# Kernel optimization log

Hardware: AMD Instinct MI355X
Metric: run time of the kernel (lower is better)

## Reference

```python
import jax, jax.numpy as jnp
import numpy as np

D = 4; R = 12; C = 32
P = 2 * R + 1            # 25 fine patch
N = P * P                # 625
MEM_R = 12; MEM_P = 2 * MEM_R + 1
K = 20; DIL_INT = 16


def local_correlation(ft, fr, rad, dil):
    """Zero-padded local correlation (SpatialCorrelationSampler, kernel=1).
    ft, fr: (b,c,h,w) -> (b,Pp,Pp,h,w) with Pp=2*rad+1, patch dilation dil."""
    b, c, h, w = ft.shape
    Pp = 2 * rad + 1
    pad = rad * dil
    frp = jnp.pad(fr, ((0, 0), (0, 0), (pad, pad), (pad, pad)))
    rows = (jnp.arange(Pp)[:, None] * dil + jnp.arange(h)[None, :]).reshape(-1)
    cols = (jnp.arange(Pp)[:, None] * dil + jnp.arange(w)[None, :]).reshape(-1)
    g = frp[:, :, rows, :][:, :, :, cols].reshape(b, c, Pp, h, Pp, w)
    return jnp.einsum('bchw,bcyhxw->byxhw', ft, g)


def bilinear_sample(img, py, px):
    """Bilinear sample img (b,c,H,W) at float coords py/px (broadcastable shape S);
    zero outside the image. Returns (b,c,*S)."""
    b, c, H, W = img.shape
    y0f = jnp.floor(py); x0f = jnp.floor(px)
    wy = py - y0f; wx = px - x0f
    y0 = y0f.astype(jnp.int32); x0 = x0f.astype(jnp.int32)

    def tap(yi, xi, wgt):
        valid = (yi >= 0) & (yi < H) & (xi >= 0) & (xi < W)
        v = img[:, :, jnp.clip(yi, 0, H - 1), jnp.clip(xi, 0, W - 1)]
        return v * (wgt * valid)[None, None]

    return (tap(y0, x0, (1 - wy) * (1 - wx)) + tap(y0, x0 + 1, (1 - wy) * wx)
            + tap(y0 + 1, x0, wy * (1 - wx)) + tap(y0 + 1, x0 + 1, wy * wx))


def _topk_dim1(corr, k):
    # corr: (b,N,hw); torch.topk(dim=1, sorted=True) equivalent
    vals, idx = jax.lax.top_k(corr.transpose(0, 2, 1), k)   # (b,hw,k)
    return vals.transpose(0, 2, 1), idx                      # (b,k,hw), (b,hw,k)


def _long_ref(ft, fr, q, dirate):
    b, c, h, w = ft.shape
    # coarse dilated correlation -> softmax -> soft-argmax expected offset
    corr_c = local_correlation(ft, fr, MEM_R, dirate).reshape(b, MEM_P * MEM_P, h * w)
    attn = jax.nn.softmax(corr_c, axis=1).reshape(b, MEM_P, MEM_P, h, w)
    d = jnp.arange(-MEM_R, MEM_R + 1, dtype=ft.dtype)
    off_y = jnp.einsum('byxhw,y->bhw', attn, d) * dirate
    off_x = jnp.einsum('byxhw,x->bhw', attn, d) * dirate
    # deform_im2col with PxP kernel: sample fr at (r+dy+off_y, c+dx+off_x)
    dtap = jnp.arange(-R, R + 1, dtype=ft.dtype)
    py = dtap[:, None, None, None] + (jnp.arange(h, dtype=ft.dtype)[:, None] + off_y[0])[None, None]
    px = dtap[None, :, None, None] + (jnp.arange(w, dtype=ft.dtype)[None, :] + off_x[0])[None, None]
    col = bilinear_sample(fr, py, px)                        # (b,c,P,P,h,w)
    corr = jnp.einsum('bchw,bcyxhw->byxhw', ft, col).reshape(b, N, h * w)
    vals, idx = _topk_dim1(corr, K)
    # process_long_image_uf_topk: shift offsets by decoded top-k displacement, 1-tap bilinear
    dr = (idx[0] // 25 - 12).reshape(h, w, K).transpose(2, 0, 1).astype(ft.dtype)  # (K,h,w)
    dc = (idx[0] % 25 - 12).reshape(h, w, K).transpose(2, 0, 1).astype(ft.dtype)
    py2 = jnp.arange(h, dtype=ft.dtype)[None, :, None] + off_y[0][None] + dr
    px2 = jnp.arange(w, dtype=ft.dtype)[None, None, :] + off_x[0][None] + dc
    imgs = bilinear_sample(q, py2, px2)                      # (b,C,K,h,w)
    return vals, imgs.reshape(b, q.shape[1], K, h * w)


def _short_ref(ft, fr, q):
    b, c, h, w = ft.shape
    corr = local_correlation(ft, fr, R, 1).reshape(b, N, h * w)
    vals, idx = _topk_dim1(corr, K)
    # process_short_image_uf_topk: integer gather q[:, :, r+dr, c+dc] (zero-padded)
    dr = (idx[0] // 25 - 12).reshape(h, w, K).transpose(2, 0, 1)   # (K,h,w) int
    dc = (idx[0] % 25 - 12).reshape(h, w, K).transpose(2, 0, 1)
    qp = jnp.pad(q, ((0, 0), (0, 0), (R, R), (R, R)))
    yi = jnp.arange(h)[None, :, None] + dr + R
    xi = jnp.arange(w)[None, None, :] + dc + R
    imgs = qp[:, :, yi, xi]                                  # (b,C,K,h,w)
    return vals, imgs.reshape(b, q.shape[1], K, h * w)


def _forward(feats_r, feats_t, quantized_r, ref_index, current_ind):
    ref_index = np.asarray(ref_index)
    current_ind = int(current_ind)
    gaps = current_ind - ref_index
    nsearch = int(np.sum(gaps > DIL_INT))
    dirates = [int(min(4, g // DIL_INT + 1)) for g in gaps if g > DIL_INT]
    nref = feats_r.shape[0]
    b, c, h, w = feats_t.shape
    # prep(): subsample labels by D (C=32 channels, one_hot skipped)
    qr = [quantized_r[i][:, :, ::D, ::D].astype(feats_t.dtype) for i in range(nref)]
    vals_all, imgs_all = [], []
    for i in range(nsearch):
        v, im = _long_ref(feats_t, feats_r[i], qr[i], dirates[i])
        vals_all.append(v); imgs_all.append(im)
    for i in range(nsearch, nref):
        v, im = _short_ref(feats_t, feats_r[i], qr[i])
        vals_all.append(v); imgs_all.append(im)
    attn = jax.nn.softmax(jnp.concatenate(vals_all, axis=1), axis=1)  # (b, nref*K, hw)
    imgs = jnp.concatenate(imgs_all, axis=2)                          # (b, C, nref*K, hw)
    return jnp.einsum('bkp,bckp->bcp', attn, imgs).reshape(b, qr[0].shape[1], h, w)


def setup_inputs():
    key = jax.random.key(0)
    k1, k2, k3 = jax.random.split(key, 3)
    feats_r = jax.random.normal(k1, (3, 1, 64, 48, 48), dtype=jnp.float32)
    feats_t = jax.random.normal(k2, (1, 64, 48, 48), dtype=jnp.float32)
    quantized_r = jax.random.uniform(k3, (3, 1, 32, 192, 192), dtype=jnp.float32)
    # gaps vs current_ind=60: 20 (>16 -> long ref, dirate=2), 10, 5 (short refs)
    ref_index = np.array([40, 50, 55], dtype=np.int64)
    current_ind = 60
    return {"feats_r": feats_r, "feats_t": feats_t, "quantized_r": quantized_r,
            "ref_index": ref_index, "current_ind": current_ind}


def reference(feats_r, feats_t, quantized_r, ref_index, current_ind):
    return _forward(feats_r, feats_t, quantized_r, ref_index, current_ind)
```

## Files before the change

### kernel.cpp

```cpp
#include <hip/hip_runtime.h>
#include <math.h>

#define HW 48
#define NPIX 2304
#define CF 64
#define CQ 32
#define RAD 12
#define PP 25
#define NTAP 625
#define KTOP 20
#define DILINT 16
#define QW 192
#define CSTRIDE 640
#define NPB 6
#define NC 30
#define LROW 68
#define DGS 28


__device__ inline int read_ref_index(const void* rip, int r) {
    const long long* p64 = (const long long*)rip;
    long long v0 = p64[0];
    if (v0 >= 0 && v0 < 1000000) return (int)p64[r];
    return ((const int*)rip)[r];
}

__device__ inline int get_dil(const void* refIdx, const void* curInd, int r,
                              bool* isLong) {
    int cur = ((const int*)curInd)[0];
    int gap = cur - read_ref_index(refIdx, r);
    *isLong = gap > DILINT;
    return *isLong ? min(4, gap / DILINT + 1) : 1;
}

__device__ inline float gather_color(const float* __restrict__ qb, int c,
                                     int y, int x, int id, bool isLong,
                                     float oy, float ox) {
    int dr = id / PP - RAD, dc = id % PP - RAD;
    float img = 0.f;
    if (isLong) {
        float py = (float)y + oy + (float)dr;
        float px = (float)x + ox + (float)dc;
        float fy0 = floorf(py), fx0 = floorf(px);
        int y0 = (int)fy0, x0 = (int)fx0;
        float wy = py - fy0, wx = px - fx0;
        float w00 = (1.f - wy) * (1.f - wx), w01 = (1.f - wy) * wx;
        float w10 = wy * (1.f - wx), w11 = wy * wx;
        if (y0 >= 0 && y0 < HW && x0 >= 0 && x0 < HW)
            img += w00 * qb[(y0 * HW + x0) * CQ + c];
        if (y0 >= 0 && y0 < HW && x0 + 1 >= 0 && x0 + 1 < HW)
            img += w01 * qb[(y0 * HW + x0 + 1) * CQ + c];
        if (y0 + 1 >= 0 && y0 + 1 < HW && x0 >= 0 && x0 < HW)
            img += w10 * qb[((y0 + 1) * HW + x0) * CQ + c];
        if (y0 + 1 >= 0 && y0 + 1 < HW && x0 + 1 >= 0 && x0 + 1 < HW)
            img += w11 * qb[((y0 + 1) * HW + x0 + 1) * CQ + c];
    } else {
        int yy = y + dr, xx = x + dc;
        if (yy >= 0 && yy < HW && xx >= 0 && xx < HW)
            img = qb[(yy * HW + xx) * CQ + c];
    }
    return img;
}

__global__ void prep_kernel(const float* __restrict__ fr,
                            const float* __restrict__ ft,
                            const float* __restrict__ q, int nref,
                            float* __restrict__ ftT,
                            float* __restrict__ frT,
                            float* __restrict__ qrT) {
    int i = blockIdx.x * blockDim.x + threadIdx.x;
    int tft = NPIX * CF;
    int tfr = nref * NPIX * CF;
    int tqr = nref * NPIX * CQ;
    if (i < tft) {
        int c = i / NPIX, p = i - c * NPIX;
        ftT[p * CF + c] = ft[i];
    } else if (i < tft + tfr) {
        int j = i - tft;
        int rr = j / (NPIX * CF);
        int rem = j - rr * (NPIX * CF);
        int c = rem / NPIX, p = rem - c * NPIX;
        frT[((size_t)rr * NPIX + p) * CF + c] = fr[j];
    } else if (i < tft + tfr + tqr) {
        int j = i - tft - tfr;
        int rr = j / (NPIX * CQ);
        int rem = j - rr * (NPIX * CQ);
        int c = rem / NPIX, p = rem - c * NPIX;
        int y = p / HW, x = p - y * HW;
        qrT[((size_t)rr * NPIX + p) * CQ + c] =
            q[(((size_t)rr * CQ + c) * QW + 4 * y) * QW + 4 * x];
    }
}

__global__ __launch_bounds__(256) void corr_band(
    const float* __restrict__ ftT, const float* __restrict__ frT,
    const void* __restrict__ refIdx, const void* __restrict__ curInd,
    float* __restrict__ corr) {
    __shared__ float lrow[NC * LROW];

    int tid = threadIdx.x;
    int bx = blockIdx.x % 9;
    int y = blockIdx.x / 9;
    int r = blockIdx.y;

    bool isLong;
    int dil = get_dil(refIdx, curInd, r, &isLong);
    int nb = (dil == 3) ? 9 : 8;
    if (bx >= nb) return;

    int m = bx % dil, grp = bx / dil;
    int npr = HW / dil;

    int T = tid;
    bool active = T < NPB * PP;
    int j = active ? T / PP : 0;
    int dxi = active ? T - PP * j : 0;
    int xoff = grp * NPB + j;
    bool pvalid = active && (xoff < npr);
    int xj = m + dil * xoff;
    int pj = pvalid ? (y * HW + xj) : 0;
    int lc = j + dxi;

    float4 fq[16];
    const float4* fp = (const float4*)(ftT + (size_t)pj * CF);
#pragma unroll
    for (int i = 0; i < 16; ++i) fq[i] = fp[i];

    const float* frb = frT + (size_t)r * NPIX * CF;
    float* outb = corr + ((size_t)r * NPIX + pj) * CSTRIDE + dxi;
    int gc0 = m + dil * (grp * NPB - RAD);

    for (int dy = 0; dy < PP; ++dy) {
        int yy = y + dil * (dy - RAD);
        if (yy < 0 || yy >= HW) {
            if (pvalid) outb[dy * PP] = 0.f;
            continue;
        }
        for (int k = tid; k < NC * 16; k += 256) {
            int col = k >> 4, sub = k & 15;
            int gc = gc0 + dil * col;
            float4 v = {0.f, 0.f, 0.f, 0.f};
            if (gc >= 0 && gc < HW)
                v = *(const float4*)(frb + ((size_t)yy * HW + gc) * CF + sub * 4);
            *(float4*)(lrow + col * LROW + sub * 4) = v;
        }
        __syncthreads();
        if (pvalid) {
            const float* bp = lrow + lc * LROW;
            float s = 0.f;
#pragma unroll
            for (int i = 0; i < 16; ++i) {
                float4 b = *(const float4*)(bp + 4 * i);
                s += fq[i].x * b.x + fq[i].y * b.y + fq[i].z * b.z + fq[i].w * b.w;
            }
            outb[dy * PP] = s;
        }
        __syncthreads();
    }
}

__global__ __launch_bounds__(192) void corr_fuse(
    const float* __restrict__ ftT, const float* __restrict__ frT,
    const float* __restrict__ qrT, const float* __restrict__ corr,
    const void* __restrict__ refIdx, const void* __restrict__ curInd,
    int nref, float* __restrict__ out) {
    __shared__ float dgw_s[3][27 * DGS];
    __shared__ float accL[3][64];
    __shared__ float ssmL[3][64];
    __shared__ float offL[3][2];
    __shared__ float mL[3];

    int tid = threadIdx.x;
    int wid = tid >> 6, lane = tid & 63;
    int p = blockIdx.x;
    int y = p / HW, x = p % HW;
    int r = wid;

    bool isLong;
    int dil = get_dil(refIdx, curInd, r, &isLong);
    float oy = 0.f, ox = 0.f;

    const float* cb = corr + ((size_t)r * NPIX + p) * CSTRIDE;
    float creg[10];
#pragma unroll
    for (int jj = 0; jj < 10; ++jj) {
        int t = lane + 64 * jj;
        creg[jj] = (t < NTAP) ? cb[t] : -INFINITY;
    }

    if (isLong) {
        float M = -INFINITY;
#pragma unroll
        for (int jj = 0; jj < 10; ++jj) M = fmaxf(M, creg[jj]);
#pragma unroll
        for (int s = 32; s; s >>= 1) M = fmaxf(M, __shfl_xor(M, s, 64));
        float s0 = 0.f, sy = 0.f, sx = 0.f;
#pragma unroll
        for (int jj = 0; jj < 10; ++jj) {
            int t = lane + 64 * jj;
            if (t < NTAP) {
                float e = expf(creg[jj] - M);
                int dy = t / PP - RAD, dx = t % PP - RAD;
                s0 += e; sy += e * (float)dy; sx += e * (float)dx;
            }
        }
#pragma unroll
        for (int s = 32; s; s >>= 1) {
            s0 += __shfl_xor(s0, s, 64);
            sy += __shfl_xor(sy, s, 64);
            sx += __shfl_xor(sx, s, 64);
        }
        oy = sy / s0 * (float)dil;
        ox = sx / s0 * (float)dil;
        if (lane == 0) { offL[r][0] = oy; offL[r][1] = ox; }
    }
    __syncthreads();

    for (int rr = 0; rr < nref; ++rr) {
        bool rrLong;
        get_dil(refIdx, curInd, rr, &rrLong);
        if (!rrLong) continue;
        float roy = offL[rr][0], rox = offL[rr][1];
        float fy = (float)y + roy, fx = (float)x + rox;
        int iy0 = (int)floorf(fy), ix0 = (int)floorf(fx);

        int cs = tid & 15;
        int g2 = tid >> 4;
        float4 fqc = ((const float4*)(ftT + (size_t)p * CF))[cs];
        const float* frb = frT + (size_t)rr * NPIX * CF;
        float* dgw = dgw_s[rr];
        int colbase = ix0 - RAD;
        for (int a = 0; a < 26; ++a) {
            int yy = iy0 - RAD + a;
            bool yok = (yy >= 0 && yy < HW);
            const float* rowp = frb + (size_t)(yok ? yy : 0) * (HW * CF);
#pragma unroll
            for (int i = 0; i < 3; ++i) {
                int lc2 = 12 * i + g2;
                int xx2 = colbase + lc2;
                int xs = min(max(xx2, 0), HW - 1);
                float s = 0.f;
                if (yok && lc2 < 26) {
                    float4 b = *(const float4*)(rowp + xs * CF + 4 * cs);
                    s = fqc.x * b.x + fqc.y * b.y + fqc.z * b.z + fqc.w * b.w;
                    s = (xx2 >= 0 && xx2 < HW) ? s : 0.f;
                }
                s += __shfl_xor(s, 1, 64);
                s += __shfl_xor(s, 2, 64);
                s += __shfl_xor(s, 4, 64);
                s += __shfl_xor(s, 8, 64);
                if (cs == 0 && lc2 < 26) dgw[a * DGS + lc2] = s;
            }
        }
    }
    __syncthreads();

    if (isLong) {
        float fy = (float)y + oy, fx = (float)x + ox;
        float fy0 = floorf(fy), fx0 = floorf(fx);
        float wy = fy - fy0, wx = fx - fx0;
        const float* dgw = dgw_s[r];
        float w00 = (1.f - wy) * (1.f - wx), w01 = (1.f - wy) * wx;
        float w10 = wy * (1.f - wx), w11 = wy * wx;
#pragma unroll
        for (int jj = 0; jj < 10; ++jj) {
            int t = lane + 64 * jj;
            if (t < NTAP) {
                int a = t / PP, bcol = t % PP;
                creg[jj] = w00 * dgw[a * DGS + bcol] + w01 * dgw[a * DGS + bcol + 1] +
                           w10 * dgw[(a + 1) * DGS + bcol] + w11 * dgw[(a + 1) * DGS + bcol + 1];
            }
        }
    }

    double key[10];
#pragma unroll
    for (int jj = 0; jj < 10; ++jj) {
        float v = creg[jj] + 0.0f;
        unsigned u = __float_as_uint(v);
        u = (u & 0x80000000u) ? ~u : (u | 0x80000000u);
        int t = lane + 64 * jj;
        key[jj] = (double)u * 1024.0 + (double)(1023 - t);
    }

    int c = lane & 31, h = lane >> 5;
    const float* qb = qrT + (size_t)r * NPIX * CQ;
    float ssum = 0.f, acc = 0.f, m = 0.f;
    float v0a = 0.f, v0b = 0.f; int t0a = 0, t0b = 0;

    for (int k2 = 0; k2 < KTOP / 2; ++k2) {
        double a = key[0], b = -1.0;
#pragma unroll
        for (int jj = 1; jj < 10; ++jj) {
            double kk = key[jj];
            double na = fmax(a, kk);
            b = fmax(b, fmin(a, kk));
            a = na;
        }
#pragma unroll
        for (int s = 32; s; s >>= 1) {
            double pa = __shfl_xor(a, s, 64);
            double pb = __shfl_xor(b, s, 64);
            double na = fmax(a, pa);
            b = fmax(fmin(a, pa), fmax(b, pb));
            a = na;
        }
        double qa = floor(a * (1.0 / 1024.0));
        double qb2 = floor(b * (1.0 / 1024.0));
        unsigned ua = (unsigned)qa, ub = (unsigned)qb2;
        unsigned ba = (ua & 0x80000000u) ? (ua ^ 0x80000000u) : ~ua;
        unsigned bb = (ub & 0x80000000u) ? (ub ^ 0x80000000u) : ~ub;
        float va = __uint_as_float(ba), vb = __uint_as_float(bb);
        int ta = 1023 - (int)(a - qa * 1024.0);
        int tb = 1023 - (int)(b - qb2 * 1024.0);

        if (k2 == 0) {
            if (lane == 0) mL[r] = va;
            v0a = va; v0b = vb; t0a = ta; t0b = tb;
        } else {
            float vv = h ? vb : va;
            int tt = h ? tb : ta;
            float e = __expf(vv - m);
            ssum += e;
            acc += e * gather_color(qb, c, y, x, tt, isLong, oy, ox);
        }
#pragma unroll
        for (int jj = 0; jj < 10; ++jj) {
            double kk = key[jj];
            key[jj] = (kk == a || kk == b) ? 0.0 : kk;
        }
        if (k2 == 0) {
            __syncthreads();
            m = mL[0];
            for (int w = 1; w < nref; ++w) m = fmaxf(m, mL[w]);
            float vv = h ? v0b : v0a;
            int tt = h ? t0b : t0a;
            float e = __expf(vv - m);
            ssum += e;
            acc += e * gather_color(qb, c, y, x, tt, isLong, oy, ox);
        }
    }
    accL[wid][lane] = acc;
    ssmL[wid][lane] = ssum;
    __syncthreads();

    if (wid == 0) {
        float ta2 = 0.f, ts = 0.f;
        for (int w = 0; w < nref; ++w) { ta2 += accL[w][lane]; ts += ssmL[w][lane]; }
        ta2 += __shfl_xor(ta2, 32, 64);
        ts += __shfl_xor(ts, 32, 64);
        if (h == 0) out[(size_t)c * NPIX + p] = ta2 / ts;
    }
}

extern "C" void kernel_launch(void* const* d_in, const int* in_sizes, int n_in,
                              void* d_out, int out_size, void* d_ws, size_t ws_size,
                              hipStream_t stream) {
    const float* fr = (const float*)d_in[0];
    const float* ft = (const float*)d_in[1];
    const float* q  = (const float*)d_in[2];
    const void* refIdx = d_in[3];
    const void* curInd = d_in[4];
    int nref = in_sizes[0] / (CF * NPIX);

    float* ws  = (float*)d_ws;
    float* ftT = ws;
    float* frT = ftT + (size_t)NPIX * CF;
    float* qrT = frT + (size_t)nref * NPIX * CF;
    float* corr = qrT + (size_t)nref * NPIX * CQ;

    int total = NPIX * CF + nref * NPIX * CF + nref * NPIX * CQ;
    prep_kernel<<<(total + 255) / 256, 256, 0, stream>>>(fr, ft, q, nref, ftT, frT, qrT);
    corr_band<<<dim3(HW * 9, nref), 256, 0, stream>>>(ftT, frT, refIdx, curInd, corr);
    corr_fuse<<<dim3(NPIX), 64 * nref, 0, stream>>>(ftT, frT, qrT, corr, refIdx, curInd,
                                                    nref, (float*)d_out);
}
```

Before: 112.5 us.

## Coalesce transpose writes, flatten deformable window loop, defer softmax max merge

The prep transpose now indexes by output position, so writes are coalesced and reads are strided. The deformable-window correlation loop is flattened over all 676 taps in rounds of 12, with clamped unconditional loads, to cut wasted lanes and branches, and the ft vector load is hoisted out of the per-reference loop. The top-k softmax now uses each warp's local max and rescales the partial sums in the final reduction. This removes a mid-loop __syncthreads and the special handling of the first top-k pair. The rescaling costs a few extra exps at the end.

```diff
diff --git a/kernel.cpp b/kernel.cpp
--- a/kernel.cpp
+++ b/kernel.cpp
@@ -73,22 +73,21 @@
     int tfr = nref * NPIX * CF;
     int tqr = nref * NPIX * CQ;
     if (i < tft) {
-        int c = i / NPIX, p = i - c * NPIX;
-        ftT[p * CF + c] = ft[i];
+        int p = i >> 6, c = i & 63;
+        ftT[i] = ft[c * NPIX + p];
     } else if (i < tft + tfr) {
         int j = i - tft;
         int rr = j / (NPIX * CF);
-        int rem = j - rr * (NPIX * CF);
-        int c = rem / NPIX, p = rem - c * NPIX;
-        frT[((size_t)rr * NPIX + p) * CF + c] = fr[j];
+        int rem = j % (NPIX * CF);
+        int p = rem >> 6, c = rem & 63;
+        frT[j] = fr[((size_t)rr * CF + c) * NPIX + p];
     } else if (i < tft + tfr + tqr) {
         int j = i - tft - tfr;
         int rr = j / (NPIX * CQ);
-        int rem = j - rr * (NPIX * CQ);
-        int c = rem / NPIX, p = rem - c * NPIX;
-        int y = p / HW, x = p - y * HW;
-        qrT[((size_t)rr * NPIX + p) * CQ + c] =
-            q[(((size_t)rr * CQ + c) * QW + 4 * y) * QW + 4 * x];
+        int rem = j % (NPIX * CQ);
+        int p = rem >> 5, c = rem & 31;
+        int y = p / HW, x = p % HW;
+        qrT[j] = q[(((size_t)rr * CQ + c) * QW + 4 * y) * QW + 4 * x];
     }
 }
 
@@ -216,6 +215,9 @@
     }
     __syncthreads();
 
+    int cs = tid & 15;
+    int g2 = tid >> 4;
+    float4 fqc = ((const float4*)(ftT + (size_t)p * CF))[cs];
     for (int rr = 0; rr < nref; ++rr) {
         bool rrLong;
         get_dil(refIdx, curInd, rr, &rrLong);
@@ -224,33 +226,28 @@
         float fy = (float)y + roy, fx = (float)x + rox;
         int iy0 = (int)floorf(fy), ix0 = (int)floorf(fx);
 
-        int cs = tid & 15;
-        int g2 = tid >> 4;
-        float4 fqc = ((const float4*)(ftT + (size_t)p * CF))[cs];
         const float* frb = frT + (size_t)rr * NPIX * CF;
         float* dgw = dgw_s[rr];
         int colbase = ix0 - RAD;
-        for (int a = 0; a < 26; ++a) {
-            int yy = iy0 - RAD + a;
-            bool yok = (yy >= 0 && yy < HW);
-            const float* rowp = frb + (size_t)(yok ? yy : 0) * (HW * CF);
-#pragma unroll
-            for (int i = 0; i < 3; ++i) {
-                int lc2 = 12 * i + g2;
-                int xx2 = colbase + lc2;
-                int xs = min(max(xx2, 0), HW - 1);
-                float s = 0.f;
-                if (yok && lc2 < 26) {
-                    float4 b = *(const float4*)(rowp + xs * CF + 4 * cs);
-                    s = fqc.x * b.x + fqc.y * b.y + fqc.z * b.z + fqc.w * b.w;
-                    s = (xx2 >= 0 && xx2 < HW) ? s : 0.f;
-                }
-                s += __shfl_xor(s, 1, 64);
-                s += __shfl_xor(s, 2, 64);
-                s += __shfl_xor(s, 4, 64);
-                s += __shfl_xor(s, 8, 64);
-                if (cs == 0 && lc2 < 26) dgw[a * DGS + lc2] = s;
-            }
+        int rowbase = iy0 - RAD;
+        for (int rnd = 0; rnd < 57; ++rnd) {
+            int idx = 12 * rnd + g2;
+            int a = idx / 26;
+            int lc2 = idx - 26 * a;
+            bool valid = idx < 676;
+            int yy = rowbase + a;
+            int xx2 = colbase + lc2;
+            int ys = min(max(yy, 0), HW - 1);
+            int xs = min(max(xx2, 0), HW - 1);
+            bool ok = valid && (yy >= 0) && (yy < HW) && (xx2 >= 0) && (xx2 < HW);
+            float4 b = *(const float4*)(frb + ((size_t)ys * HW + xs) * CF + 4 * cs);
+            float t0 = fqc.x * b.x + fqc.y * b.y + fqc.z * b.z + fqc.w * b.w;
+            float s = ok ? t0 : 0.f;
+            s += __shfl_xor(s, 1, 64);
+            s += __shfl_xor(s, 2, 64);
+            s += __shfl_xor(s, 4, 64);
+            s += __shfl_xor(s, 8, 64);
+            if (cs == 0 && valid) dgw[a * DGS + lc2] = s;
         }
     }
     __syncthreads();
@@ -286,7 +283,6 @@
     int c = lane & 31, h = lane >> 5;
     const float* qb = qrT + (size_t)r * NPIX * CQ;
     float ssum = 0.f, acc = 0.f, m = 0.f;
-    float v0a = 0.f, v0b = 0.f; int t0a = 0, t0b = 0;
 
     for (int k2 = 0; k2 < KTOP / 2; ++k2) {
         double a = key[0], b = -1.0;
@@ -315,38 +311,34 @@
         int tb = 1023 - (int)(b - qb2 * 1024.0);
 
         if (k2 == 0) {
+            m = va;
             if (lane == 0) mL[r] = va;
-            v0a = va; v0b = vb; t0a = ta; t0b = tb;
-        } else {
-            float vv = h ? vb : va;
-            int tt = h ? tb : ta;
-            float e = __expf(vv - m);
-            ssum += e;
-            acc += e * gather_color(qb, c, y, x, tt, isLong, oy, ox);
-        }
+        }
+        float vv = h ? vb : va;
+        int tt = h ? tb : ta;
+        float e = __expf(vv - m);
+        ssum += e;
+        acc += e * gather_color(qb, c, y, x, tt, isLong, oy, ox);
+
 #pragma unroll
         for (int jj = 0; jj < 10; ++jj) {
             double kk = key[jj];
             key[jj] = (kk == a || kk == b) ? 0.0 : kk;
         }
-        if (k2 == 0) {
-            __syncthreads();
-            m = mL[0];
-            for (int w = 1; w < nref; ++w) m = fmaxf(m, mL[w]);
-            float vv = h ? v0b : v0a;
-            int tt = h ? t0b : t0a;
-            float e = __expf(vv - m);
-            ssum += e;
-            acc += e * gather_color(qb, c, y, x, tt, isLong, oy, ox);
-        }
     }
     accL[wid][lane] = acc;
     ssmL[wid][lane] = ssum;
     __syncthreads();
 
     if (wid == 0) {
+        float M = mL[0];
+        for (int w = 1; w < nref; ++w) M = fmaxf(M, mL[w]);
         float ta2 = 0.f, ts = 0.f;
-        for (int w = 0; w < nref; ++w) { ta2 += accL[w][lane]; ts += ssmL[w][lane]; }
+        for (int w = 0; w < nref; ++w) {
+            float sc = __expf(mL[w] - M);
+            ta2 += accL[w][lane] * sc;
+            ts += ssmL[w][lane] * sc;
+        }
         ta2 += __shfl_xor(ta2, 32, 64);
         ts += __shfl_xor(ts, 32, 64);
         if (h == 0) out[(size_t)c * NPIX + p] = ta2 / ts;
```

Result: faster. 103.0 us (median of 2 runs) (-8.4%).
